# Optimization experiments

Hardware: AMD Instinct MI355X
Metric: run time of the kernel (lower is better)

The kernel has to match this reference:

```python
import jax, jax.numpy as jnp
import numpy as np

DIM = 1024
SEQ = 4096


def setup_inputs() -> dict:
    key = jax.random.key(0)
    ks = jax.random.split(key, 7)
    s = 1.0 / np.sqrt(DIM)
    return {
        "X": jax.random.normal(ks[0], (SEQ, DIM), dtype=jnp.float32),
        "Wq": jax.random.uniform(ks[1], (DIM, DIM), jnp.float32, -s, s),
        "bq": jax.random.uniform(ks[2], (DIM,), jnp.float32, -s, s),
        "Wk": jax.random.uniform(ks[3], (DIM, DIM), jnp.float32, -s, s),
        "bk": jax.random.uniform(ks[4], (DIM,), jnp.float32, -s, s),
        "Wv": jax.random.uniform(ks[5], (DIM, DIM), jnp.float32, -s, s),
        "bv": jax.random.uniform(ks[6], (DIM,), jnp.float32, -s, s),
    }


def reference(X, Wq, bq, Wk, bk, Wv, bv):
    # QKV projections (nn.Linear: x @ W.T + b); here W stored as [in, out]
    Q = X @ Wq + bq            # [S, D]
    K = X @ Wk + bk            # [S, D]
    V = X @ Wv + bv            # [S, D]
    scale = 1.0 / jnp.sqrt(jnp.asarray(X.shape[-1], X.dtype))
    scores = (Q @ K.T) * scale  # [S, S]
    attn = jax.nn.softmax(scores, axis=-1)
    return attn @ V            # [S, D]
```

## Files before the change

### kernel.cpp

```cpp
#include <hip/hip_runtime.h>

typedef unsigned short u16;
typedef unsigned int u32;
typedef __bf16 bf16x8 __attribute__((ext_vector_type(8)));
typedef float f32x4 __attribute__((ext_vector_type(4)));
typedef u16 u16x4 __attribute__((ext_vector_type(4)));

__device__ __forceinline__ u16 f32_to_bf16(float f) {
    u32 u = __builtin_bit_cast(u32, f);
    u32 r = (u + 0x7fffu + ((u >> 16) & 1u)) >> 16;
    return (u16)r;
}

__device__ __forceinline__ float bf16_to_f32(u16 h) {
    u32 u = (u32)h << 16;
    return __builtin_bit_cast(float, u);
}

__device__ __forceinline__ void async_cp16(const u16* g, u16* l) {
    __builtin_amdgcn_global_load_lds(
        (const __attribute__((address_space(1))) u32*)g,
        (__attribute__((address_space(3))) u32*)l, 16, 0, 0);
}

#define GEMM_PROLOG(Aptr, Bptr, LDA, LDB)                                     \
    __shared__ u16 lds[16384];                                                \
    const int tid  = threadIdx.x;                                             \
    const int wid  = tid >> 6;                                                \
    const int lane = tid & 63;                                                \
    const int s0 = wid * 2, s1 = s0 + 1;                                      \
    const int rr = lane >> 2;                                                 \
    const int cc = (lane & 3) * 8;                                            \
    const u16* gA0 = (Aptr) + (size_t)(bm + s0 * 16 + rr) * (LDA) + cc;       \
    const u16* gA1 = (Aptr) + (size_t)(bm + s1 * 16 + rr) * (LDA) + cc;      \
    const u16* gB0 = (Bptr) + (size_t)(bn + s0 * 16 + rr) * (LDB) + cc;       \
    const u16* gB1 = (Bptr) + (size_t)(bn + s1 * 16 + rr) * (LDB) + cc;       \
    u16* lA0  = &lds[s0 * 512];                                               \
    u16* lA1  = &lds[s1 * 512];                                               \
    u16* lA0h = lA0 + 4096;                                                   \
    u16* lA1h = lA1 + 4096;                                                   \
    u16* lB0  = &lds[8192 + s0 * 512];                                        \
    u16* lB1  = &lds[8192 + s1 * 512];                                        \
    u16* lB0h = lB0 + 4096;                                                   \
    u16* lB1h = lB1 + 4096;                                                   \
    const int wm = (wid >> 1) * 64;                                           \
    const int wn = (wid & 1) * 64;                                            \
    const int row16 = lane & 15;                                              \
    const int quad  = lane >> 4;                                              \
    f32x4 acc[4][4];                                                          \
    const f32x4 zero = {0.f, 0.f, 0.f, 0.f};                                  \
    _Pragma("unroll")                                                         \
    for (int i = 0; i < 4; i++)                                               \
        _Pragma("unroll")                                                     \
        for (int j = 0; j < 4; j++) acc[i][j] = zero;

#define GEMM_KLOOP(KLEN)                                                      \
    for (int kt = 0; kt < (KLEN); kt += 64) {                                 \
        __syncthreads();                                                      \
        async_cp16(gA0, lA0);                                                 \
        async_cp16(gA1, lA1);                                                 \
        async_cp16(gA0 + 32, lA0h);                                           \
        async_cp16(gA1 + 32, lA1h);                                           \
        async_cp16(gB0, lB0);                                                 \
        async_cp16(gB1, lB1);                                                 \
        async_cp16(gB0 + 32, lB0h);                                           \
        async_cp16(gB1 + 32, lB1h);                                           \
        gA0 += 64; gA1 += 64; gB0 += 64; gB1 += 64;                           \
        __syncthreads();                                                      \
        _Pragma("unroll")                                                     \
        for (int h = 0; h < 2; h++) {                                         \
            bf16x8 fa[4], fb[4];                                              \
            _Pragma("unroll")                                                 \
            for (int im = 0; im < 4; im++)                                    \
                fa[im] = *(const bf16x8*)&lds[h * 4096 + (wm + im * 16 + row16) * 32 + quad * 8]; \
            _Pragma("unroll")                                                 \
            for (int in = 0; in < 4; in++)                                    \
                fb[in] = *(const bf16x8*)&lds[8192 + h * 4096 + (wn + in * 16 + row16) * 32 + quad * 8]; \
            _Pragma("unroll")                                                 \
            for (int im = 0; im < 4; im++)                                    \
                _Pragma("unroll")                                             \
                for (int in = 0; in < 4; in++)                                \
                    acc[im][in] = __builtin_amdgcn_mfma_f32_16x16x32_bf16(    \
                        fa[im], fb[in], acc[im][in], 0, 0, 0);                \
        }                                                                     \
    }

#define SWIZZLE_2D()                                                          \
    const int L   = blockIdx.x;                                               \
    const int id2 = L & 255;                                                  \
    const int bm  = (((id2 & 7) * 4) + (id2 >> 6)) * 128;                     \
    const int bn  = (((id2 >> 3) & 7) + (L >> 8) * 8) * 128;

__global__ __launch_bounds__(256, 4)
void gemm_qkv(const u16* __restrict__ A, const u16* __restrict__ B,
              u16* __restrict__ C, u16* __restrict__ Vt,
              const float* __restrict__ bias,
              int K, int lda, int ldb, int ldc)
{
    SWIZZLE_2D()
    GEMM_PROLOG(A, B, lda, ldb)
    GEMM_KLOOP(K)
    if (bn < 2048) {
        #pragma unroll
        for (int im = 0; im < 4; im++) {
            #pragma unroll
            for (int in = 0; in < 4; in++) {
                const int n = bn + wn + in * 16 + row16;
                const float bv = bias[n];
                #pragma unroll
                for (int r = 0; r < 4; r++) {
                    const int m = bm + wm + im * 16 + quad * 4 + r;
                    C[(size_t)m * ldc + n] = f32_to_bf16(acc[im][in][r] + bv);
                }
            }
        }
    } else {
        #pragma unroll
        for (int im = 0; im < 4; im++) {
            #pragma unroll
            for (int in = 0; in < 4; in++) {
                const int n = bn + wn + in * 16 + row16;
                const float bv = bias[n];
                const int d = n - 2048;
                const int m = bm + wm + im * 16 + quad * 4;
                u16x4 pk;
                #pragma unroll
                for (int r = 0; r < 4; r++)
                    pk[r] = f32_to_bf16(acc[im][in][r] + bv);
                *(u16x4*)&Vt[(size_t)d * 4096 + m] = pk;
            }
        }
    }
}

__global__ __launch_bounds__(256, 4)
void gemm_score_exp(const u16* __restrict__ A, const u16* __restrict__ B,
                    u16* __restrict__ P, float* __restrict__ rowsum,
                    int K, int lda, int ldb, int ldc, float scale)
{
    SWIZZLE_2D()
    GEMM_PROLOG(A, B, lda, ldb)
    GEMM_KLOOP(K)
    #pragma unroll
    for (int im = 0; im < 4; im++) {
        #pragma unroll
        for (int r = 0; r < 4; r++) {
            const int m = bm + wm + im * 16 + quad * 4 + r;
            float rs = 0.f;
            #pragma unroll
            for (int in = 0; in < 4; in++) {
                const int n = bn + wn + in * 16 + row16;
                float e = __expf(acc[im][in][r] * scale);
                P[(size_t)m * ldc + n] = f32_to_bf16(e);
                rs += e;
            }
            rs += __shfl_xor(rs, 1);
            rs += __shfl_xor(rs, 2);
            rs += __shfl_xor(rs, 4);
            rs += __shfl_xor(rs, 8);
            if (row16 == 0) atomicAdd(&rowsum[m], rs);
        }
    }
}

__global__ __launch_bounds__(256, 4)
void gemm_pv_splitk(const u16* __restrict__ A, const u16* __restrict__ B,
                    u16* __restrict__ P0, u16* __restrict__ P1,
                    u16* __restrict__ P2, u16* __restrict__ P3,
                    int Kq, int lda, int ldb, int ldc)
{
    const int id2 = blockIdx.x;
    const int bm  = (((id2 & 7) * 4) + (id2 >> 6)) * 128;
    const int bn  = ((id2 >> 3) & 7) * 128;
    const int z   = blockIdx.y;
    u16* C = (z == 0) ? P0 : (z == 1) ? P1 : (z == 2) ? P2 : P3;
    const int koff = z * Kq;
    GEMM_PROLOG(A + koff, B + koff, lda, ldb)
    GEMM_KLOOP(Kq)
    #pragma unroll
    for (int im = 0; im < 4; im++) {
        #pragma unroll
        for (int in = 0; in < 4; in++) {
            const int n = bn + wn + in * 16 + row16;
            #pragma unroll
            for (int r = 0; r < 4; r++) {
                const int m = bm + wm + im * 16 + quad * 4 + r;
                C[(size_t)m * ldc + n] = f32_to_bf16(acc[im][in][r]);
            }
        }
    }
}

__global__ __launch_bounds__(256)
void reduce4_scale(float4* __restrict__ out, const u16x4* __restrict__ p0,
                   const u16x4* __restrict__ p1, const u16x4* __restrict__ p2,
                   const u16x4* __restrict__ p3, const float* __restrict__ rowsum)
{
    const int i = blockIdx.x * 256 + threadIdx.x;
    const float inv = 1.0f / rowsum[i >> 8];
    u16x4 a = p0[i], b = p1[i], c = p2[i], d = p3[i];
    float4 o;
    o.x = (bf16_to_f32(a[0]) + bf16_to_f32(b[0]) + bf16_to_f32(c[0]) + bf16_to_f32(d[0])) * inv;
    o.y = (bf16_to_f32(a[1]) + bf16_to_f32(b[1]) + bf16_to_f32(c[1]) + bf16_to_f32(d[1])) * inv;
    o.z = (bf16_to_f32(a[2]) + bf16_to_f32(b[2]) + bf16_to_f32(c[2]) + bf16_to_f32(d[2])) * inv;
    o.w = (bf16_to_f32(a[3]) + bf16_to_f32(b[3]) + bf16_to_f32(c[3]) + bf16_to_f32(d[3])) * inv;
    out[i] = o;
}

__global__ __launch_bounds__(256)
void prep_all(const float4* __restrict__ X, uint2* __restrict__ Xb,
              const float* __restrict__ W0, const float* __restrict__ W1,
              const float* __restrict__ W2, u16* __restrict__ Wt,
              const float* __restrict__ bq, const float* __restrict__ bk,
              const float* __restrict__ bv, float* __restrict__ b3,
              float* __restrict__ rowsum)
{
    __shared__ float t[32][33];
    const int b = blockIdx.x;
    if (b < 4096) {
        const int i = b * 256 + threadIdx.x;
        float4 v = X[i];
        uint2 o;
        o.x = (u32)f32_to_bf16(v.x) | ((u32)f32_to_bf16(v.y) << 16);
        o.y = (u32)f32_to_bf16(v.z) | ((u32)f32_to_bf16(v.w) << 16);
        Xb[i] = o;
    } else if (b < 7168) {
        const int tt = b - 4096;
        const int z  = tt >> 10;
        const int r  = tt & 1023;
        const float* W = (z == 0) ? W0 : (z == 1) ? W1 : W2;
        u16* dst = Wt + (size_t)z * 1024 * 1024;
        const int bk2 = (r & 31) * 32;
        const int bn2 = (r >> 5) * 32;
        const int tx = threadIdx.x & 31;
        const int ty = threadIdx.x >> 5;
        #pragma unroll
        for (int i = 0; i < 32; i += 8)
            t[ty + i][tx] = W[(size_t)(bk2 + ty + i) * 1024 + bn2 + tx];
        __syncthreads();
        #pragma unroll
        for (int i = 0; i < 32; i += 8)
            dst[(size_t)(bn2 + ty + i) * 1024 + bk2 + tx] = f32_to_bf16(t[tx][ty + i]);
    } else {
        const int i = (b - 7168) * 256 + threadIdx.x;
        if (i < 3072)
            b3[i] = (i < 1024) ? bq[i] : (i < 2048) ? bk[i - 1024] : bv[i - 2048];
        else
            rowsum[i - 3072] = 0.f;
    }
}

extern "C" void kernel_launch(void* const* d_in, const int* in_sizes, int n_in,
                              void* d_out, int out_size, void* d_ws, size_t ws_size,
                              hipStream_t stream)
{
    const float* X  = (const float*)d_in[0];
    const float* Wq = (const float*)d_in[1];
    const float* bq = (const float*)d_in[2];
    const float* Wk = (const float*)d_in[3];
    const float* bk = (const float*)d_in[4];
    const float* Wv = (const float*)d_in[5];
    const float* bv = (const float*)d_in[6];
    float* out = (float*)d_out;

    char* ws = (char*)d_ws;
    u16*   P      = (u16*)ws;
    u16*   Xb     = (u16*)ws;
    u16*   WqkvT  = (u16*)(ws + (8u << 20));
    float* rowsum = (float*)(ws + (32u << 20));
    float* bias3  = (float*)(ws + (32u << 20) + (64u << 10));
    u16*   QKV    = (u16*)(ws + (33u << 20));
    u16*   p0     = (u16*)(ws + (33u << 20));
    u16*   p1     = (u16*)(ws + (41u << 20));
    u16*   p2     = (u16*)(ws + (49u << 20));
    u16*   p3     = (u16*)(ws + (57u << 20));
    u16*   Vt     = (u16*)(ws + (65u << 20));

    prep_all<<<7196, 256, 0, stream>>>((const float4*)X, (uint2*)Xb,
        Wq, Wk, Wv, WqkvT, bq, bk, bv, bias3, rowsum);

    gemm_qkv<<<768, 256, 0, stream>>>(Xb, WqkvT, QKV, Vt, bias3,
        1024, 1024, 1024, 3072);

    gemm_score_exp<<<1024, 256, 0, stream>>>(QKV, QKV + 1024, P, rowsum,
        1024, 3072, 3072, 4096, 0.03125f);

    gemm_pv_splitk<<<dim3(256, 4), 256, 0, stream>>>(P, Vt, p0, p1, p2, p3,
        1024, 4096, 4096, 1024);

    reduce4_scale<<<4096, 256, 0, stream>>>((float4*)out, (const u16x4*)p0,
        (const u16x4*)p1, (const u16x4*)p2, (const u16x4*)p3, rowsum);
}
```

Measured before the change: 206.5 us.

## Rewrite GEMM core with 256x256 tiles, double-buffered async LDS loads, swizzled layout

```diff
diff --git a/kernel.cpp b/kernel.cpp
--- a/kernel.cpp
+++ b/kernel.cpp
@@ -23,106 +23,161 @@
         (__attribute__((address_space(3))) u32*)l, 16, 0, 0);
 }
 
-#define GEMM_PROLOG(Aptr, Bptr, LDA, LDB)                                     \
-    __shared__ u16 lds[16384];                                                \
+#define G2_DECL(Aptr, Bptr, LDA, LDB, KLEN)                                   \
+    __shared__ u16 lds[65536];                                                \
     const int tid  = threadIdx.x;                                             \
     const int wid  = tid >> 6;                                                \
     const int lane = tid & 63;                                                \
-    const int s0 = wid * 2, s1 = s0 + 1;                                      \
-    const int rr = lane >> 2;                                                 \
-    const int cc = (lane & 3) * 8;                                            \
-    const u16* gA0 = (Aptr) + (size_t)(bm + s0 * 16 + rr) * (LDA) + cc;       \
-    const u16* gA1 = (Aptr) + (size_t)(bm + s1 * 16 + rr) * (LDA) + cc;      \
-    const u16* gB0 = (Bptr) + (size_t)(bn + s0 * 16 + rr) * (LDB) + cc;       \
-    const u16* gB1 = (Bptr) + (size_t)(bn + s1 * 16 + rr) * (LDB) + cc;       \
-    u16* lA0  = &lds[s0 * 512];                                               \
-    u16* lA1  = &lds[s1 * 512];                                               \
-    u16* lA0h = lA0 + 4096;                                                   \
-    u16* lA1h = lA1 + 4096;                                                   \
-    u16* lB0  = &lds[8192 + s0 * 512];                                        \
-    u16* lB1  = &lds[8192 + s1 * 512];                                        \
-    u16* lB0h = lB0 + 4096;                                                   \
-    u16* lB1h = lB1 + 4096;                                                   \
-    const int wm = (wid >> 1) * 64;                                           \
-    const int wn = (wid & 1) * 64;                                            \
+    const int wr = wid >> 2;                 \
+    const int wc = wid & 3;                  \
     const int row16 = lane & 15;                                              \
     const int quad  = lane >> 4;                                              \
-    f32x4 acc[4][4];                                                          \
-    const f32x4 zero = {0.f, 0.f, 0.f, 0.f};                                  \
+    const int sc0 = (quad * 8) ^ ((row16 & 7) * 8);       \
+    const int gr = lane >> 3;                           \
+    const int gc = ((lane & 7) ^ gr) * 8;               \
+    const int blk0 = wid * 2, blk1 = blk0 + 1;                                \
+    const size_t ldaS = (LDA), ldbS = (LDB);                                  \
+    const u16* gA = (Aptr) + (size_t)(bm + gr) * ldaS + gc;                   \
+    const u16* gB = (Bptr) + (size_t)(bn + gr) * ldbS + gc;                   \
+    const int NT = (KLEN) >> 6;                                               \
+    f32x4 acc[8][4];                                                          \
+    {                                                                         \
+        const f32x4 z_ = {0.f, 0.f, 0.f, 0.f};                                \
+        _Pragma("unroll")                                                     \
+        for (int i_ = 0; i_ < 8; i_++)                                        \
+            _Pragma("unroll")                                                 \
+            for (int j_ = 0; j_ < 4; j_++) acc[i_][j_] = z_;                  \
+    }
+
+#define G2_STAGE(bsel) {                                                      \
+    u16* l_ = &lds[(bsel) * 32768];                                           \
+    async_cp16(gA + (size_t)(blk0 * 8) * ldaS,       l_ + blk0 * 512);        \
+    async_cp16(gA + (size_t)(blk1 * 8) * ldaS,       l_ + blk1 * 512);        \
+    async_cp16(gA + (size_t)(128 + blk0 * 8) * ldaS, l_ + 8192 + blk0 * 512); \
+    async_cp16(gA + (size_t)(128 + blk1 * 8) * ldaS, l_ + 8192 + blk1 * 512); \
+    async_cp16(gB + (size_t)(blk0 * 8) * ldbS,       l_ + 16384 + blk0 * 512);\
+    async_cp16(gB + (size_t)(blk1 * 8) * ldbS,       l_ + 16384 + blk1 * 512);\
+    async_cp16(gB + (size_t)(128 + blk0 * 8) * ldbS, l_ + 24576 + blk0 * 512);\
+    async_cp16(gB + (size_t)(128 + blk1 * 8) * ldbS, l_ + 24576 + blk1 * 512);\
+    gA += 64; gB += 64; }
+
+#define G2_LA(cb, im, sc) \
+    (*(const bf16x8*)&lds[(cb) + wr * 8192 + (im) * 1024 + row16 * 64 + (sc)])
+#define G2_LB(cb, in, sc) \
+    (*(const bf16x8*)&lds[(cb) + 16384 + wc * 4096 + (in) * 1024 + row16 * 64 + (sc)])
+
+#define G2_MMA(IM0, JN0, FB)                                                  \
     _Pragma("unroll")                                                         \
-    for (int i = 0; i < 4; i++)                                               \
-        _Pragma("unroll")                                                     \
-        for (int j = 0; j < 4; j++) acc[i][j] = zero;
-
-#define GEMM_KLOOP(KLEN)                                                      \
-    for (int kt = 0; kt < (KLEN); kt += 64) {                                 \
-        __syncthreads();                                                      \
-        async_cp16(gA0, lA0);                                                 \
-        async_cp16(gA1, lA1);                                                 \
-        async_cp16(gA0 + 32, lA0h);                                           \
-        async_cp16(gA1 + 32, lA1h);                                           \
-        async_cp16(gB0, lB0);                                                 \
-        async_cp16(gB1, lB1);                                                 \
-        async_cp16(gB0 + 32, lB0h);                                           \
-        async_cp16(gB1 + 32, lB1h);                                           \
-        gA0 += 64; gA1 += 64; gB0 += 64; gB1 += 64;                           \
-        __syncthreads();                                                      \
-        _Pragma("unroll")                                                     \
-        for (int h = 0; h < 2; h++) {                                         \
-            bf16x8 fa[4], fb[4];                                              \
-            _Pragma("unroll")                                                 \
-            for (int im = 0; im < 4; im++)                                    \
-                fa[im] = *(const bf16x8*)&lds[h * 4096 + (wm + im * 16 + row16) * 32 + quad * 8]; \
-            _Pragma("unroll")                                                 \
-            for (int in = 0; in < 4; in++)                                    \
-                fb[in] = *(const bf16x8*)&lds[8192 + h * 4096 + (wn + in * 16 + row16) * 32 + quad * 8]; \
-            _Pragma("unroll")                                                 \
-            for (int im = 0; im < 4; im++)                                    \
-                _Pragma("unroll")                                             \
-                for (int in = 0; in < 4; in++)                                \
-                    acc[im][in] = __builtin_amdgcn_mfma_f32_16x16x32_bf16(    \
-                        fa[im], fb[in], acc[im][in], 0, 0, 0);                \
-        }                                                                     \
-    }
-
-#define SWIZZLE_2D()                                                          \
-    const int L   = blockIdx.x;                                               \
-    const int id2 = L & 255;                                                  \
-    const int bm  = (((id2 & 7) * 4) + (id2 >> 6)) * 128;                     \
-    const int bn  = (((id2 >> 3) & 7) + (L >> 8) * 8) * 128;
-
-__global__ __launch_bounds__(256, 4)
+    for (int i_m = 0; i_m < 4; i_m++)                                         \
+        _Pragma("unroll")                                                     \
+        for (int j_n = 0; j_n < 2; j_n++) {                                   \
+            acc[(IM0) + i_m][(JN0) + j_n] =                                   \
+                __builtin_amdgcn_mfma_f32_16x16x32_bf16(                      \
+                    fa[i_m][0], FB[j_n][0], acc[(IM0) + i_m][(JN0) + j_n],    \
+                    0, 0, 0);                                                 \
+            acc[(IM0) + i_m][(JN0) + j_n] =                                   \
+                __builtin_amdgcn_mfma_f32_16x16x32_bf16(                      \
+                    fa[i_m][1], FB[j_n][1], acc[(IM0) + i_m][(JN0) + j_n],    \
+                    0, 0, 0);                                                 \
+        }
+
+#define G2_KLOOP()                                                            \
+    G2_STAGE(0)                                                               \
+    G2_STAGE(1)                                                               \
+    for (int t = 0; t < NT; t++) {                                            \
+        const int cb = (t & 1) * 32768;                                       \
+        if (t < NT - 1) { asm volatile("s_waitcnt vmcnt(8)" ::: "memory"); }  \
+        else            { asm volatile("s_waitcnt vmcnt(0)" ::: "memory"); }  \
+        __builtin_amdgcn_s_barrier();                                         \
+        bf16x8 fa[4][2], f0[2][2], f1[2][2];                                  \
+                                 \
+        _Pragma("unroll")                                                     \
+        for (int i = 0; i < 4; i++) {                                         \
+            fa[i][0] = G2_LA(cb, i, sc0);                                     \
+            fa[i][1] = G2_LA(cb, i, sc0 ^ 32);                                \
+        }                                                                     \
+        _Pragma("unroll")                                                     \
+        for (int j = 0; j < 2; j++) {                                         \
+            f0[j][0] = G2_LB(cb, j, sc0);                                     \
+            f0[j][1] = G2_LB(cb, j, sc0 ^ 32);                                \
+        }                                                                     \
+        __builtin_amdgcn_s_barrier();                                         \
+        __builtin_amdgcn_s_setprio(1);                                        \
+        G2_MMA(0, 0, f0)                                                      \
+        __builtin_amdgcn_s_setprio(0);                                        \
+        __builtin_amdgcn_s_barrier();                                         \
+                                           \
+        _Pragma("unroll")                                                     \
+        for (int j = 0; j < 2; j++) {                                         \
+            f1[j][0] = G2_LB(cb, 2 + j, sc0);                                 \
+            f1[j][1] = G2_LB(cb, 2 + j, sc0 ^ 32);                            \
+        }                                                                     \
+        __builtin_amdgcn_s_barrier();                                         \
+        __builtin_amdgcn_s_setprio(1);                                        \
+        G2_MMA(0, 2, f1)                                                      \
+        __builtin_amdgcn_s_setprio(0);                                        \
+        __builtin_amdgcn_s_barrier();                                         \
+                               \
+        _Pragma("unroll")                                                     \
+        for (int i = 0; i < 4; i++) {                                         \
+            fa[i][0] = G2_LA(cb, 4 + i, sc0);                                 \
+            fa[i][1] = G2_LA(cb, 4 + i, sc0 ^ 32);                            \
+        }                                                                     \
+        __builtin_amdgcn_s_barrier();                                         \
+        __builtin_amdgcn_s_setprio(1);                                        \
+        G2_MMA(4, 2, f1)                                                      \
+        __builtin_amdgcn_s_setprio(0);                                        \
+        __builtin_amdgcn_s_barrier();                                         \
+                                    \
+        _Pragma("unroll")                                                     \
+        for (int j = 0; j < 2; j++) {                                         \
+            f0[j][0] = G2_LB(cb, j, sc0);                                     \
+            f0[j][1] = G2_LB(cb, j, sc0 ^ 32);                                \
+        }                                                                     \
+        __builtin_amdgcn_s_barrier();                                         \
+        __builtin_amdgcn_s_setprio(1);                                        \
+        G2_MMA(4, 0, f0)                                                      \
+        __builtin_amdgcn_s_setprio(0);                                        \
+        asm volatile("s_waitcnt lgkmcnt(0)" ::: "memory");                    \
+        __builtin_amdgcn_s_barrier();                                         \
+        if (t + 2 < NT) { G2_STAGE((t & 1)) }                                 \
+    }
+
+__global__ __launch_bounds__(512, 2)
 void gemm_qkv(const u16* __restrict__ A, const u16* __restrict__ B,
               u16* __restrict__ C, u16* __restrict__ Vt,
               const float* __restrict__ bias,
               int K, int lda, int ldb, int ldc)
 {
-    SWIZZLE_2D()
-    GEMM_PROLOG(A, B, lda, ldb)
-    GEMM_KLOOP(K)
+    const int L  = blockIdx.x;
+    const int wg = (L & 7) * 24 + (L >> 3);
+    const int bm = (wg / 12) * 256;
+    const int bn = (wg % 12) * 256;
+    G2_DECL(A, B, lda, ldb, K)
+    G2_KLOOP()
     if (bn < 2048) {
         #pragma unroll
-        for (int im = 0; im < 4; im++) {
+        for (int im = 0; im < 8; im++) {
             #pragma unroll
             for (int in = 0; in < 4; in++) {
-                const int n = bn + wn + in * 16 + row16;
+                const int n = bn + wc * 64 + in * 16 + row16;
                 const float bv = bias[n];
                 #pragma unroll
                 for (int r = 0; r < 4; r++) {
-                    const int m = bm + wm + im * 16 + quad * 4 + r;
+                    const int m = bm + wr * 128 + im * 16 + quad * 4 + r;
                     C[(size_t)m * ldc + n] = f32_to_bf16(acc[im][in][r] + bv);
                 }
             }
         }
     } else {
         #pragma unroll
-        for (int im = 0; im < 4; im++) {
+        for (int im = 0; im < 8; im++) {
             #pragma unroll
             for (int in = 0; in < 4; in++) {
-                const int n = bn + wn + in * 16 + row16;
+                const int n = bn + wc * 64 + in * 16 + row16;
                 const float bv = bias[n];
                 const int d = n - 2048;
-                const int m = bm + wm + im * 16 + quad * 4;
+                const int m = bm + wr * 128 + im * 16 + quad * 4;
                 u16x4 pk;
                 #pragma unroll
                 for (int r = 0; r < 4; r++)
@@ -133,23 +188,26 @@
     }
 }
 
-__global__ __launch_bounds__(256, 4)
+__global__ __launch_bounds__(512, 2)
 void gemm_score_exp(const u16* __restrict__ A, const u16* __restrict__ B,
                     u16* __restrict__ P, float* __restrict__ rowsum,
                     int K, int lda, int ldb, int ldc, float scale)
 {
-    SWIZZLE_2D()
-    GEMM_PROLOG(A, B, lda, ldb)
-    GEMM_KLOOP(K)
+    const int L = blockIdx.x;
+    const int xcd = L & 7, q = L >> 3;
+    const int bm = ((xcd >> 1) * 4 + (q >> 3)) * 256;
+    const int bn = ((xcd & 1) * 8 + (q & 7)) * 256;
+    G2_DECL(A, B, lda, ldb, K)
+    G2_KLOOP()
     #pragma unroll
-    for (int im = 0; im < 4; im++) {
+    for (int im = 0; im < 8; im++) {
         #pragma unroll
         for (int r = 0; r < 4; r++) {
-            const int m = bm + wm + im * 16 + quad * 4 + r;
+            const int m = bm + wr * 128 + im * 16 + quad * 4 + r;
             float rs = 0.f;
             #pragma unroll
             for (int in = 0; in < 4; in++) {
-                const int n = bn + wn + in * 16 + row16;
+                const int n = bn + wc * 64 + in * 16 + row16;
                 float e = __expf(acc[im][in][r] * scale);
                 P[(size_t)m * ldc + n] = f32_to_bf16(e);
                 rs += e;
@@ -163,28 +221,29 @@
     }
 }
 
-__global__ __launch_bounds__(256, 4)
+__global__ __launch_bounds__(512, 2)
 void gemm_pv_splitk(const u16* __restrict__ A, const u16* __restrict__ B,
                     u16* __restrict__ P0, u16* __restrict__ P1,
                     u16* __restrict__ P2, u16* __restrict__ P3,
                     int Kq, int lda, int ldb, int ldc)
 {
-    const int id2 = blockIdx.x;
-    const int bm  = (((id2 & 7) * 4) + (id2 >> 6)) * 128;
-    const int bn  = ((id2 >> 3) & 7) * 128;
-    const int z   = blockIdx.y;
+    const int L = blockIdx.x;
+    const int xcd = L & 7, q = L >> 3;
+    const int bm = ((xcd >> 1) * 4 + (q & 3)) * 256;
+    const int bn = ((xcd & 1) * 2 + (q >> 2)) * 256;
+    const int z  = blockIdx.y;
     u16* C = (z == 0) ? P0 : (z == 1) ? P1 : (z == 2) ? P2 : P3;
     const int koff = z * Kq;
-    GEMM_PROLOG(A + koff, B + koff, lda, ldb)
-    GEMM_KLOOP(Kq)
+    G2_DECL(A + koff, B + koff, lda, ldb, Kq)
+    G2_KLOOP()
     #pragma unroll
-    for (int im = 0; im < 4; im++) {
+    for (int im = 0; im < 8; im++) {
         #pragma unroll
         for (int in = 0; in < 4; in++) {
-            const int n = bn + wn + in * 16 + row16;
+            const int n = bn + wc * 64 + in * 16 + row16;
             #pragma unroll
             for (int r = 0; r < 4; r++) {
-                const int m = bm + wm + im * 16 + quad * 4 + r;
+                const int m = bm + wr * 128 + im * 16 + quad * 4 + r;
                 C[(size_t)m * ldc + n] = f32_to_bf16(acc[im][in][r]);
             }
         }
@@ -279,13 +338,13 @@
     prep_all<<<7196, 256, 0, stream>>>((const float4*)X, (uint2*)Xb,
         Wq, Wk, Wv, WqkvT, bq, bk, bv, bias3, rowsum);
 
-    gemm_qkv<<<768, 256, 0, stream>>>(Xb, WqkvT, QKV, Vt, bias3,
+    gemm_qkv<<<192, 512, 0, stream>>>(Xb, WqkvT, QKV, Vt, bias3,
         1024, 1024, 1024, 3072);
 
-    gemm_score_exp<<<1024, 256, 0, stream>>>(QKV, QKV + 1024, P, rowsum,
+    gemm_score_exp<<<256, 512, 0, stream>>>(QKV, QKV + 1024, P, rowsum,
         1024, 3072, 3072, 4096, 0.03125f);
 
-    gemm_pv_splitk<<<dim3(256, 4), 256, 0, stream>>>(P, Vt, p0, p1, p2, p3,
+    gemm_pv_splitk<<<dim3(64, 4), 512, 0, stream>>>(P, Vt, p0, p1, p2, p3,
         1024, 4096, 4096, 1024);
 
     reduce4_scale<<<4096, 256, 0, stream>>>((float4*)out, (const u16x4*)p0,
```

Measured after the change: 222.3 us. +7.7%, slower.
